# Kernel tuning notes

Measured on AMD Instinct MI355X. Metric: run time of the kernel, lower is better.

The kernel has to match this reference:

```python
import jax, jax.numpy as jnp
import numpy as np

HEADS, DK, DV = 8, 64, 64
DM = HEADS * DK                 # 512
ROUNDS, SEQ, BUCKET = 2, 4096, 64
NCHUNK = SEQ // BUCKET          # 64 chunks
NBUCKETS = SEQ // BUCKET        # 64 hash buckets (Reformer convention)
SCALE = 8.0                     # sqrt(d_k)
NEG_BIG = -1e15
BATCH = 4


def setup_inputs() -> dict:
    key = jax.random.key(0)
    kq, kk, kv, kr = jax.random.split(key, 4)
    q = jax.random.normal(kq, (BATCH, SEQ, DM), jnp.float32)
    k = jax.random.normal(kk, (BATCH, SEQ, DM), jnp.float32)
    v = jax.random.normal(kv, (BATCH, SEQ, DM), jnp.float32)
    # angular-LSH random rotations: (rounds, d_model, n_buckets//2)
    R = jax.random.normal(kr, (ROUNDS, DM, NBUCKETS // 2), jnp.float32)
    return {"q": q, "k": k, "v": v, "R": R}


def _window(x):
    # x: (r, b, S, ...) -> (r, b, n_chunks, 2*BUCKET, ...)
    # each window = [previous chunk (wrapped), current chunk]
    r, b, S = x.shape[:3]
    xc = x.reshape((r, b, NCHUNK, BUCKET) + x.shape[3:])
    return jnp.concatenate([jnp.roll(xc, 1, axis=2), xc], axis=3)


def _lsh_attention(q, k, v, R):
    b = q.shape[0]
    # --- hash queries (same sorted_idx reused for q, k, v, as in the module) ---
    rot = jnp.einsum('bsd,rdm->rbsm', q, R)                       # (r,b,S,nb/2)
    h = jnp.argmax(jnp.concatenate([rot, -rot], axis=-1), axis=-1)
    h = h.astype(jnp.int32) + 1                                    # bucket 0 reserved for padding
    sorted_idx = jnp.argsort(h, axis=-1, stable=True)              # (r,b,S)

    def gather(x):  # (b,S,d) -> (r,b,S,d) sorted by bucket per round
        xb = jnp.broadcast_to(x[None], (ROUNDS,) + x.shape)
        return jnp.take_along_axis(xb, sorted_idx[..., None], axis=2)

    qs, ks, vs = gather(q), gather(k), gather(v)
    hs = jnp.take_along_axis(h, sorted_idx, axis=2)                # (r,b,S)

    # --- chunk into local windows ---
    qs = _window(qs.reshape(ROUNDS, b, SEQ, HEADS, DK))            # (r,b,n,2c,h,dk)
    ks = _window(ks.reshape(ROUNDS, b, SEQ, HEADS, DK))
    vs = _window(vs.reshape(ROUNDS, b, SEQ, HEADS, DV))
    hw = _window(hs)                                               # (r,b,n,2c)

    # --- per-window attention with bucket mask + log-count bias ---
    attn = jnp.einsum('rbnqhd,rbnkhd->rbnhqk', qs, ks) / SCALE     # (r,b,n,h,2c,2c)
    hm = (hw[:, :, :, :, None] == hw[:, :, :, None, :]) & (hw[:, :, :, :, None] != 0)
    hm = hm[:, :, :, None].astype(jnp.float32)                     # (r,b,n,1,2c,2c)
    cnt = hm * jnp.sum(hm, axis=4, keepdims=True)                  # count term (sum over q dim, as in source)
    bias = (1.0 - hm) * NEG_BIG - jnp.log(jnp.clip(cnt, 1.0))
    attn = attn + bias
    attn = attn + jnp.eye(2 * BUCKET, dtype=attn.dtype) * -1e5     # self-attention mask
    attn = jax.nn.softmax(attn, axis=-1)
    out = jnp.einsum('rbnhml,rbnlhd->rbnmhd', attn, vs)            # (r,b,n,2c,h,dv)
    out = out[:, :, :, BUCKET:]                                    # keep current-chunk queries
    out = out.reshape(ROUNDS, b, SEQ, HEADS, DV)

    # --- unsort back to original token order, sum over rounds ---
    inv = jnp.argsort(sorted_idx, axis=-1, stable=True)
    out = jnp.take_along_axis(out, inv[:, :, :, None, None], axis=2)
    return jnp.sum(out, axis=0)                                    # (b,S,heads,dv)


def reference(q, k, v, R):
    return _lsh_attention(q, k, v, R)
```

## Files before the change

### kernel.cpp

```cpp
#include <hip/hip_runtime.h>
#include <hip/hip_bf16.h>
#include <hip/hip_fp16.h>

#define HEADS 8
#define DK 64
#define DV 64
#define DM 512
#define ROUNDS 2
#define SEQ 4096
#define BUCKET 64
#define NCHUNK 64
#define BATCH 4
#define GAP_THRESH 0.02f

typedef _Float16 f16;
typedef f16 f16x4 __attribute__((ext_vector_type(4)));
typedef f16 f16x8 __attribute__((ext_vector_type(8)));
typedef float f32x4 __attribute__((ext_vector_type(4)));

#define MFMA16(a, b, c) __builtin_amdgcn_mfma_f32_16x16x32_f16((a), (b), (c), 0, 0, 0)

__global__ __launch_bounds__(256) void hash_approx_kernel(
    const float* __restrict__ q, const float* __restrict__ R,
    int* __restrict__ h_out, unsigned char* __restrict__ flag) {
  int blk = blockIdx.x;
  int stile = blk & 63;
  int b = (blk >> 6) & (BATCH - 1);
  int r = blk >> 8;
  int s0 = stile << 6;
  int rb = r * BATCH + b;

  __shared__ f16 Rh[32 * 520];
  __shared__ f16 Rl[32 * 520];

  int tid = threadIdx.x;
  int w = tid >> 6, lane = tid & 63, lo = lane & 15, hi = lane >> 4;

  const float* rbase = R + (size_t)r * DM * 32;
#pragma unroll
  for (int i = 0; i < 16; ++i) {
    int fi = tid + i * 256;
    float4 rv = *reinterpret_cast<const float4*>(rbase + fi * 4);
    int d = fi >> 3, m0 = (fi & 7) * 4;
    const float* rp = &rv.x;
#pragma unroll
    for (int e = 0; e < 4; ++e) {
      float x = rp[e];
      f16 hx = (f16)x;
      Rh[(m0 + e) * 520 + d] = hx;
      Rl[(m0 + e) * 520 + d] = (f16)(x - (float)hx);
    }
  }
  __syncthreads();

  int qr = w * 16 + lo;
  const float* qp = q + ((size_t)b * SEQ + s0 + qr) * DM;

  f32x4 acc0 = {0.f, 0.f, 0.f, 0.f}, acc1 = {0.f, 0.f, 0.f, 0.f};
#pragma unroll 4
  for (int ks = 0; ks < 16; ++ks) {
    int k = ks * 32 + hi * 8;
    float4 a0 = *reinterpret_cast<const float4*>(qp + k);
    float4 a1 = *reinterpret_cast<const float4*>(qp + k + 4);
    float av[8] = {a0.x, a0.y, a0.z, a0.w, a1.x, a1.y, a1.z, a1.w};
    f16x8 ahi, alo;
#pragma unroll
    for (int e = 0; e < 8; ++e) {
      f16 hx = (f16)av[e];
      ahi[e] = hx;
      alo[e] = (f16)(av[e] - (float)hx);
    }
    f16x8 bh0 = *reinterpret_cast<const f16x8*>(&Rh[lo * 520 + k]);
    f16x8 bl0 = *reinterpret_cast<const f16x8*>(&Rl[lo * 520 + k]);
    f16x8 bh1 = *reinterpret_cast<const f16x8*>(&Rh[(16 + lo) * 520 + k]);
    f16x8 bl1 = *reinterpret_cast<const f16x8*>(&Rl[(16 + lo) * 520 + k]);
    acc0 = MFMA16(ahi, bh0, acc0);
    acc0 = MFMA16(ahi, bl0, acc0);
    acc0 = MFMA16(alo, bh0, acc0);
    acc1 = MFMA16(ahi, bh1, acc1);
    acc1 = MFMA16(ahi, bl1, acc1);
    acc1 = MFMA16(alo, bh1, acc1);
  }

#pragma unroll
  for (int rg = 0; rg < 4; ++rg) {
    float c0 = acc0[rg], c1 = acc1[rg];
    float v1 = c0;
    int i1 = lo;
    float v2 = -INFINITY;
    float cv[3] = {c1, -c0, -c1};
    int ci[3] = {16 + lo, 32 + lo, 48 + lo};
#pragma unroll
    for (int c = 0; c < 3; ++c) {
      if (cv[c] > v1) { v2 = v1; v1 = cv[c]; i1 = ci[c]; }
      else v2 = fmaxf(v2, cv[c]);
    }
#pragma unroll
    for (int off = 1; off <= 8; off <<= 1) {
      float ov1 = __shfl_xor(v1, off);
      int oi1 = __shfl_xor(i1, off);
      float ov2 = __shfl_xor(v2, off);
      if (ov1 > v1 || (ov1 == v1 && oi1 < i1)) {
        v2 = fmaxf(v1, ov2);
        v1 = ov1;
        i1 = oi1;
      } else {
        v2 = fmaxf(v2, ov1);
      }
    }
    if (lo == 0) {
      int grow = s0 + w * 16 + hi * 4 + rg;
      size_t gid = (size_t)rb * SEQ + grow;
      h_out[gid] = i1 + 1;
      flag[gid] = (v1 - v2 <= GAP_THRESH) ? 1 : 0;
    }
  }
}

__global__ __launch_bounds__(256) void hash_exact_kernel(
    const float* __restrict__ q, const float* __restrict__ R,
    const unsigned char* __restrict__ flag, int* __restrict__ h_out) {
  int g0 = blockIdx.x * 64;
  __shared__ int nf;
  __shared__ unsigned char list[64];
  __shared__ double pl[8][33];
  int tid = threadIdx.x;
  if (tid == 0) nf = 0;
  __syncthreads();
  if (tid < 64 && flag[g0 + tid]) {
    int idx = atomicAdd(&nf, 1);
    list[idx] = (unsigned char)tid;
  }
  __syncthreads();
  int n = nf;
  for (int i = 0; i < n; ++i) {
    int g = g0 + list[i];
    int rb = g >> 12, s = g & (SEQ - 1);
    int r = rb >> 2, b = rb & (BATCH - 1);
    int m = tid & 31, chunk = tid >> 5;
    const float* qp = q + ((size_t)b * SEQ + s) * DM;
    const float* rp = R + (size_t)r * DM * 32;
    double part = 0.0;
    for (int dd = 0; dd < 64; ++dd) {
      int d = chunk * 64 + dd;
      part = fma((double)qp[d], (double)rp[(size_t)d * 32 + m], part);
    }
    pl[chunk][m] = part;
    __syncthreads();
    if (tid < 32) {
      double sum = 0.0;
#pragma unroll
      for (int c = 0; c < 8; ++c) sum += pl[c][m];
      double v = sum;
      int ix = m;
      double nv = -sum;
      if (nv > v) { v = nv; ix = m + 32; }
      for (int off = 1; off <= 16; off <<= 1) {
        double ov = __shfl_xor(v, off);
        int oi = __shfl_xor(ix, off);
        if (ov > v || (ov == v && oi < ix)) { v = ov; ix = oi; }
      }
      if (tid == 0) h_out[g] = ix + 1;
    }
    __syncthreads();
  }
}

__global__ __launch_bounds__(256) void sort_kernel(const int* __restrict__ h,
                                                   int* __restrict__ sorted_idx) {
  int rb = blockIdx.x;
  const int* hp = h + (size_t)rb * SEQ;
  __shared__ unsigned char hs[SEQ];
  __shared__ unsigned char rs[SEQ];
  __shared__ int tile_cnt[64][64];
  __shared__ int tile_base[64][64];
  __shared__ int bucket_base[64];
  __shared__ int bucket_tot[64];
  int tid = threadIdx.x;
  int wave = tid >> 6, lane = tid & 63;
  for (int i = tid; i < 64 * 64; i += 256) ((int*)tile_cnt)[i] = 0;
  __syncthreads();
  for (int t = wave; t < 64; t += 4) {
    int s = (t << 6) + lane;
    int hv = hp[s] - 1;
    unsigned long long mm = ~0ull;
#pragma unroll
    for (int bit = 0; bit < 6; ++bit) {
      unsigned long long bb = __ballot((hv >> bit) & 1);
      mm &= ((hv >> bit) & 1) ? bb : ~bb;
    }
    int rank = __popcll(mm & ((1ull << lane) - 1ull));
    hs[s] = (unsigned char)hv;
    rs[s] = (unsigned char)rank;
    if (rank == 0) tile_cnt[t][hv] = __popcll(mm);
  }
  __syncthreads();
  if (tid < 64) {
    int bkt = tid;
    int run = 0;
    for (int t = 0; t < 64; ++t) { tile_base[t][bkt] = run; run += tile_cnt[t][bkt]; }
    bucket_tot[bkt] = run;
  }
  __syncthreads();
  if (tid == 0) {
    int run = 0;
    for (int bkt = 0; bkt < 64; ++bkt) { bucket_base[bkt] = run; run += bucket_tot[bkt]; }
  }
  __syncthreads();
  for (int t = wave; t < 64; t += 4) {
    int s = (t << 6) + lane;
    int hv = hs[s];
    int pos = bucket_base[hv] + tile_base[t][hv] + rs[s];
    sorted_idx[(size_t)rb * SEQ + pos] = s;
  }
}

__global__ __launch_bounds__(256) void attn_kernel(
    const float* __restrict__ q, const float* __restrict__ k,
    const float* __restrict__ v, const int* __restrict__ h,
    const int* __restrict__ sidx, float* __restrict__ out, int r,
    int accumulate) {
  int x = blockIdx.x;
  int hd = x & 7;
  int n = (x >> 3) & 63;
  int b = x >> 9;
  int rb = r * BATCH + b;

  __shared__ __align__(16) unsigned char smem[34816];
  __shared__ int orig_w[128];
  __shared__ int hw[128];
  f16* Qh = reinterpret_cast<f16*>(smem);
  f16* Kh = reinterpret_cast<f16*>(smem + 9216);
  const int VOFF = 17408;

  int tid = threadIdx.x;
  int wave = tid >> 6;
  int lane = tid & 63;
  int lo = lane & 15;
  int hi = lane >> 4;

  if (tid < 128) {
    int j = tid;
    int sp = (j < 64) ? ((((n + 63) & 63) << 6) + j) : ((n << 6) + (j - 64));
    int orig = sidx[(size_t)rb * SEQ + sp];
    orig_w[j] = orig;
    hw[j] = h[(size_t)rb * SEQ + orig];
  }
  __syncthreads();

  const size_t gbase = (size_t)b * SEQ * DM + hd * 64;

  float4 kreg[8], qreg[4];
#pragma unroll
  for (int t = 0; t < 8; ++t) {
    int idx = tid + t * 256;
    int j = idx >> 4, dq = idx & 15;
    kreg[t] = *reinterpret_cast<const float4*>(
        k + gbase + (size_t)orig_w[j] * DM + dq * 4);
  }
#pragma unroll
  for (int t = 0; t < 4; ++t) {
    int idx = tid + t * 256;
    int i = idx >> 4, dq = idx & 15;
    qreg[t] = *reinterpret_cast<const float4*>(
        q + gbase + (size_t)orig_w[64 + i] * DM + dq * 4);
  }
#pragma unroll
  for (int t = 0; t < 8; ++t) {
    int idx = tid + t * 256;
    int j = idx >> 4, dq = idx & 15;
    f16x4 hv = {(f16)kreg[t].x, (f16)kreg[t].y, (f16)kreg[t].z, (f16)kreg[t].w};
    *reinterpret_cast<f16x4*>(&Kh[j * 72 + dq * 4]) = hv;
  }
#pragma unroll
  for (int t = 0; t < 4; ++t) {
    int idx = tid + t * 256;
    int i = idx >> 4, dq = idx & 15;
    f16x4 hv = {(f16)qreg[t].x, (f16)qreg[t].y, (f16)qreg[t].z, (f16)qreg[t].w};
    *reinterpret_cast<f16x4*>(&Qh[i * 72 + dq * 4]) = hv;
  }
  __syncthreads();

  float4 vreg[8];
#pragma unroll
  for (int t = 0; t < 8; ++t) {
    int idx = tid + t * 256;
    int l = idx >> 4, dq = idx & 15;
    vreg[t] = *reinterpret_cast<const float4*>(
        v + gbase + (size_t)orig_w[l] * DM + dq * 4);
  }

  f32x4 acc[8];
#pragma unroll
  for (int t = 0; t < 8; ++t) acc[t] = (f32x4){0.f, 0.f, 0.f, 0.f};

  int qr_a = wave * 16 + lo;
  f16x8 aq0 = *reinterpret_cast<const f16x8*>(&Qh[qr_a * 72 + hi * 8]);
  f16x8 aq1 = *reinterpret_cast<const f16x8*>(&Qh[qr_a * 72 + 32 + hi * 8]);
#pragma unroll
  for (int t = 0; t < 8; ++t) {
    f16x8 b0 = *reinterpret_cast<const f16x8*>(&Kh[(t * 16 + lo) * 72 + hi * 8]);
    f16x8 b1 = *reinterpret_cast<const f16x8*>(&Kh[(t * 16 + lo) * 72 + 32 + hi * 8]);
    acc[t] = MFMA16(aq0, b0, acc[t]);
    acc[t] = MFMA16(aq1, b1, acc[t]);
  }

  int hq[4];
#pragma unroll
  for (int rg = 0; rg < 4; ++rg) hq[rg] = hw[64 + wave * 16 + hi * 4 + rg];
#pragma unroll
  for (int t = 0; t < 8; ++t) {
    int key = t * 16 + lo;
    int hj = hw[key];
#pragma unroll
    for (int rg = 0; rg < 4; ++rg) {
      int qr = wave * 16 + hi * 4 + rg;
      float lg = acc[t][rg] * 0.125f;
      if (hj != hq[rg]) lg = -1e15f;
      if (key == 64 + qr) lg -= 1e5f;
      acc[t][rg] = lg;
    }
  }
  float mx[4] = {-INFINITY, -INFINITY, -INFINITY, -INFINITY};
#pragma unroll
  for (int t = 0; t < 8; ++t)
#pragma unroll
    for (int rg = 0; rg < 4; ++rg) mx[rg] = fmaxf(mx[rg], acc[t][rg]);
#pragma unroll
  for (int off = 1; off <= 8; off <<= 1)
#pragma unroll
    for (int rg = 0; rg < 4; ++rg) mx[rg] = fmaxf(mx[rg], __shfl_xor(mx[rg], off));
  float sm[4] = {0.f, 0.f, 0.f, 0.f};
#pragma unroll
  for (int t = 0; t < 8; ++t)
#pragma unroll
    for (int rg = 0; rg < 4; ++rg) {
      float ev = __expf(acc[t][rg] - mx[rg]);
      acc[t][rg] = ev;
      sm[rg] += ev;
    }
#pragma unroll
  for (int off = 1; off <= 8; off <<= 1)
#pragma unroll
    for (int rg = 0; rg < 4; ++rg) sm[rg] += __shfl_xor(sm[rg], off);
  float inv[4];
#pragma unroll
  for (int rg = 0; rg < 4; ++rg) inv[rg] = 1.0f / sm[rg];

  __syncthreads();

#pragma unroll
  for (int t = 0; t < 8; ++t) {
    int key = t * 16 + lo;
#pragma unroll
    for (int rg = 0; rg < 4; ++rg) {
      int qr = wave * 16 + hi * 4 + rg;
      *reinterpret_cast<f16*>(smem + qr * 272 + key * 2) =
          (f16)(acc[t][rg] * inv[rg]);
    }
  }
#pragma unroll
  for (int t = 0; t < 8; ++t) {
    int idx = tid + t * 256;
    int l = idx >> 4, dq = idx & 15;
    const float* vp = &vreg[t].x;
#pragma unroll
    for (int c = 0; c < 4; ++c) {
      int dv = dq * 4 + c;
      int off = (l * 2 + (((dv >> 3) & 7) << 4)) & 255;
      *reinterpret_cast<f16*>(smem + VOFF + dv * 272 + off) = (f16)vp[c];
    }
  }
  __syncthreads();

  f32x4 o[4];
#pragma unroll
  for (int dt = 0; dt < 4; ++dt) o[dt] = (f32x4){0.f, 0.f, 0.f, 0.f};
#pragma unroll
  for (int lt = 0; lt < 4; ++lt) {
    f16x8 ap = *reinterpret_cast<const f16x8*>(
        smem + qr_a * 272 + lt * 64 + hi * 16);
#pragma unroll
    for (int dt = 0; dt < 4; ++dt) {
      int dvr = dt * 16 + lo;
      int off = (lt * 64 + hi * 16 + (((dvr >> 3) & 7) << 4)) & 255;
      f16x8 bv = *reinterpret_cast<const f16x8*>(smem + VOFF + dvr * 272 + off);
      o[dt] = MFMA16(ap, bv, o[dt]);
    }
  }

#pragma unroll
  for (int dt = 0; dt < 4; ++dt) {
#pragma unroll
    for (int rg = 0; rg < 4; ++rg) {
      int qr = wave * 16 + hi * 4 + rg;
      float* dst = out + gbase + (size_t)orig_w[64 + qr] * DM + dt * 16 + lo;
      if (accumulate) {
        *dst = *dst + o[dt][rg];
      } else {
        *dst = o[dt][rg];
      }
    }
  }
}

extern "C" void kernel_launch(void* const* d_in, const int* in_sizes, int n_in,
                              void* d_out, int out_size, void* d_ws,
                              size_t ws_size, hipStream_t stream) {
  (void)out_size; (void)ws_size;
  const int R_ELEMS = ROUNDS * DM * 32;
  const float *q, *k, *v, *R;
  if (n_in >= 4 && in_sizes[0] == R_ELEMS) {
    R = (const float*)d_in[0];
    k = (const float*)d_in[1];
    q = (const float*)d_in[2];
    v = (const float*)d_in[3];
  } else {
    q = (const float*)d_in[0];
    k = (const float*)d_in[1];
    v = (const float*)d_in[2];
    R = (const float*)d_in[3];
  }
  float* out = (float*)d_out;
  char* ws = (char*)d_ws;
  int* h = (int*)ws;
  int* sidx = (int*)(ws + ROUNDS * BATCH * SEQ * 4);
  unsigned char* flag = (unsigned char*)(ws + 2 * ROUNDS * BATCH * SEQ * 4);

  hash_approx_kernel<<<ROUNDS * BATCH * (SEQ / 64), 256, 0, stream>>>(q, R, h, flag);
  hash_exact_kernel<<<ROUNDS * BATCH * (SEQ / 64), 256, 0, stream>>>(q, R, flag, h);
  sort_kernel<<<ROUNDS * BATCH, 256, 0, stream>>>(h, sidx);
  attn_kernel<<<BATCH * NCHUNK * HEADS, 256, 0, stream>>>(q, k, v, h, sidx, out, 0, 0);
  attn_kernel<<<BATCH * NCHUNK * HEADS, 256, 0, stream>>>(q, k, v, h, sidx, out, 1, 1);
}
```

Before: 204.9 us.

## Fuse exact-hash fallback into approx hash kernel and merge both rounds via atomics

Folds the fp64 exact-hash recomputation for near-tie rows into the approximate hash kernel, which removes one launch and the flag buffer round-trip. The two per-round attention launches become one grid covering both rounds. Outputs are accumulated with float atomicAdd after a memset that zeroes the output first. Launch bounds for occupancy are added to two kernels. The atomics and memset add traffic, and the fp32 atomic summation order is not deterministic.

```diff
diff --git a/kernel.cpp b/kernel.cpp
--- a/kernel.cpp
+++ b/kernel.cpp
@@ -20,9 +20,9 @@
 
 #define MFMA16(a, b, c) __builtin_amdgcn_mfma_f32_16x16x32_f16((a), (b), (c), 0, 0, 0)
 
-__global__ __launch_bounds__(256) void hash_approx_kernel(
+__global__ __launch_bounds__(256, 2) void hash_approx_kernel(
     const float* __restrict__ q, const float* __restrict__ R,
-    int* __restrict__ h_out, unsigned char* __restrict__ flag) {
+    int* __restrict__ h_out) {
   int blk = blockIdx.x;
   int stile = blk & 63;
   int b = (blk >> 6) & (BATCH - 1);
@@ -32,9 +32,13 @@
 
   __shared__ f16 Rh[32 * 520];
   __shared__ f16 Rl[32 * 520];
+  __shared__ int nf;
+  __shared__ unsigned char list[64];
+  __shared__ double pl[8][33];
 
   int tid = threadIdx.x;
   int w = tid >> 6, lane = tid & 63, lo = lane & 15, hi = lane >> 4;
+  if (tid == 0) nf = 0;
 
   const float* rbase = R + (size_t)r * DM * 32;
 #pragma unroll
@@ -109,41 +113,27 @@
       }
     }
     if (lo == 0) {
-      int grow = s0 + w * 16 + hi * 4 + rg;
-      size_t gid = (size_t)rb * SEQ + grow;
+      int lrow = w * 16 + hi * 4 + rg;
+      size_t gid = (size_t)rb * SEQ + s0 + lrow;
       h_out[gid] = i1 + 1;
-      flag[gid] = (v1 - v2 <= GAP_THRESH) ? 1 : 0;
-    }
-  }
-}
-
-__global__ __launch_bounds__(256) void hash_exact_kernel(
-    const float* __restrict__ q, const float* __restrict__ R,
-    const unsigned char* __restrict__ flag, int* __restrict__ h_out) {
-  int g0 = blockIdx.x * 64;
-  __shared__ int nf;
-  __shared__ unsigned char list[64];
-  __shared__ double pl[8][33];
-  int tid = threadIdx.x;
-  if (tid == 0) nf = 0;
-  __syncthreads();
-  if (tid < 64 && flag[g0 + tid]) {
-    int idx = atomicAdd(&nf, 1);
-    list[idx] = (unsigned char)tid;
-  }
-  __syncthreads();
+      if (v1 - v2 <= GAP_THRESH) {
+        int idx = atomicAdd(&nf, 1);
+        list[idx] = (unsigned char)lrow;
+      }
+    }
+  }
+  __syncthreads();
+
   int n = nf;
   for (int i = 0; i < n; ++i) {
-    int g = g0 + list[i];
-    int rb = g >> 12, s = g & (SEQ - 1);
-    int r = rb >> 2, b = rb & (BATCH - 1);
+    int s = s0 + list[i];
     int m = tid & 31, chunk = tid >> 5;
-    const float* qp = q + ((size_t)b * SEQ + s) * DM;
-    const float* rp = R + (size_t)r * DM * 32;
+    const float* qx = q + ((size_t)b * SEQ + s) * DM;
+    const float* rx = R + (size_t)r * DM * 32;
     double part = 0.0;
     for (int dd = 0; dd < 64; ++dd) {
       int d = chunk * 64 + dd;
-      part = fma((double)qp[d], (double)rp[(size_t)d * 32 + m], part);
+      part = fma((double)qx[d], (double)rx[(size_t)d * 32 + m], part);
     }
     pl[chunk][m] = part;
     __syncthreads();
@@ -160,7 +150,7 @@
         int oi = __shfl_xor(ix, off);
         if (ov > v || (ov == v && oi < ix)) { v = ov; ix = oi; }
       }
-      if (tid == 0) h_out[g] = ix + 1;
+      if (tid == 0) h_out[(size_t)rb * SEQ + s] = ix + 1;
     }
     __syncthreads();
   }
@@ -215,15 +205,15 @@
   }
 }
 
-__global__ __launch_bounds__(256) void attn_kernel(
+__global__ __launch_bounds__(256, 4) void attn_kernel(
     const float* __restrict__ q, const float* __restrict__ k,
     const float* __restrict__ v, const int* __restrict__ h,
-    const int* __restrict__ sidx, float* __restrict__ out, int r,
-    int accumulate) {
+    const int* __restrict__ sidx, float* __restrict__ out) {
   int x = blockIdx.x;
   int hd = x & 7;
   int n = (x >> 3) & 63;
-  int b = x >> 9;
+  int b = (x >> 9) & (BATCH - 1);
+  int r = x >> 11;
   int rb = r * BATCH + b;
 
   __shared__ __align__(16) unsigned char smem[34816];
@@ -395,11 +385,7 @@
     for (int rg = 0; rg < 4; ++rg) {
       int qr = wave * 16 + hi * 4 + rg;
       float* dst = out + gbase + (size_t)orig_w[64 + qr] * DM + dt * 16 + lo;
-      if (accumulate) {
-        *dst = *dst + o[dt][rg];
-      } else {
-        *dst = o[dt][rg];
-      }
+      atomicAdd(dst, o[dt][rg]);
     }
   }
 }
@@ -425,11 +411,9 @@
   char* ws = (char*)d_ws;
   int* h = (int*)ws;
   int* sidx = (int*)(ws + ROUNDS * BATCH * SEQ * 4);
-  unsigned char* flag = (unsigned char*)(ws + 2 * ROUNDS * BATCH * SEQ * 4);
-
-  hash_approx_kernel<<<ROUNDS * BATCH * (SEQ / 64), 256, 0, stream>>>(q, R, h, flag);
-  hash_exact_kernel<<<ROUNDS * BATCH * (SEQ / 64), 256, 0, stream>>>(q, R, flag, h);
+
+  hipMemsetAsync(out, 0, (size_t)BATCH * SEQ * DM * sizeof(float), stream);
+  hash_approx_kernel<<<ROUNDS * BATCH * (SEQ / 64), 256, 0, stream>>>(q, R, h);
   sort_kernel<<<ROUNDS * BATCH, 256, 0, stream>>>(h, sidx);
-  attn_kernel<<<BATCH * NCHUNK * HEADS, 256, 0, stream>>>(q, k, v, h, sidx, out, 0, 0);
-  attn_kernel<<<BATCH * NCHUNK * HEADS, 256, 0, stream>>>(q, k, v, h, sidx, out, 1, 1);
+  attn_kernel<<<ROUNDS * BATCH * NCHUNK * HEADS, 256, 0, stream>>>(q, k, v, h, sidx, out);
 }
```

Result: slower. 214.0 us (+4.5%).
